# Kernel optimization log

Measured on AMD Instinct MI355X. Metric: run time of the kernel, lower is better.

## Reference

```python
import jax, jax.numpy as jnp
import numpy as np

B, CIN, COUT, K, H, W_SP = 16, 16, 16, 3, 384, 384


def setup_inputs() -> dict:
    key = jax.random.key(0)
    k1, k2 = jax.random.split(key)
    x = jax.random.normal(k1, (B, CIN, H, W_SP), dtype=jnp.float32)
    W = jax.random.normal(k2, (COUT, CIN, K, K), dtype=jnp.float32) * 0.05
    return {"x": x, "W": W}


def reference(x, W):
    b, cin, h, w = x.shape
    cout, _, kh, kw = W.shape
    # torch.where(x < 0, 0, 1): binary activity mask (x == 0 maps to 1)
    mask = (x >= 0).astype(x.dtype)
    # adaptive_avg_pool2d(mask, kh): h % kh == 0 and w % kw == 0, so bins are
    # exact equal-size means -> reshape + mean.  (b, cin, kh, kw)
    att = mask.reshape(b, cin, kh, h // kh, kw, w // kw).mean(axis=(3, 5))
    att = att.reshape(b, cin, kh * kw)
    att = kh * kw * jax.nn.softmax(att, axis=2) - 1.0
    att = 1.0 + jax.nn.sigmoid(att).reshape(b, cin, kh, kw)
    # per-sample modulated weights: (b, cout, cin, kh, kw); broadcast over cout
    wmod = W[None, :, :, :, :] * att[:, None, :, :, :]

    def conv_one(xi, wi):
        # xi: (cin, h, w), wi: (cout, cin, kh, kw); stride 1, padding 1 (same)
        return jax.lax.conv_general_dilated(
            xi[None], wi, window_strides=(1, 1), padding=[(1, 1), (1, 1)],
            dimension_numbers=("NCHW", "OIHW", "NCHW"))[0]

    # equivalent to the groups=b grouped-conv trick, but without materializing
    # the (1, b*cin, h, w) view
    y = jax.vmap(conv_one)(x, wmod)  # (b, cout, h, w)
    return y
```

## Files before the change

### kernel.cpp

```cpp
#include <hip/hip_runtime.h>
#include <hip/hip_bf16.h>
#include <math.h>

#define BB   16
#define CI   16
#define CO   16
#define HH   384
#define WW   384
#define HW   (HH * WW)

#define TSW 32
#define TSH 16
#define HSW 34
#define HSH 18
#define NPX (HSW * HSH)

typedef __bf16 bfx8 __attribute__((ext_vector_type(8)));
typedef float  f32x4 __attribute__((ext_vector_type(4)));

__device__ __forceinline__ uint32_t pack_bf16(float a, float b) {
  uint32_t ua = __builtin_bit_cast(uint32_t, a);
  uint32_t ub = __builtin_bit_cast(uint32_t, b);
  ua = (ua + 0x7FFFu + ((ua >> 16) & 1u)) >> 16;
  ub = (ub + 0x7FFFu + ((ub >> 16) & 1u)) >> 16;
  return ua | (ub << 16);
}

__global__ __launch_bounds__(256) void pool_kernel(
    const float* __restrict__ x, float* __restrict__ pooled) {
  const int bx = blockIdx.x;
  const int plane = bx / 9;
  const int bin = bx - plane * 9;
  const int br = (bin / 3) * 128;
  const int bc4 = (bin % 3) * 32;
  const float4* xp = (const float4*)(x + (size_t)plane * HW);
  const int tid = threadIdx.x;

  int cnt = 0;
#pragma unroll
  for (int k = 0; k < 16; ++k) {
    const int idx = tid + k * 256;
    const int r = idx >> 5;
    const int c4 = idx & 31;
    const float4 v = xp[(size_t)(br + r) * (WW / 4) + bc4 + c4];
    cnt += (v.x >= 0.f) + (v.y >= 0.f) + (v.z >= 0.f) + (v.w >= 0.f);
  }
#pragma unroll
  for (int s = 32; s > 0; s >>= 1) cnt += __shfl_down(cnt, s);

  __shared__ int wsum[4];
  const int lane = tid & 63, wid = tid >> 6;
  if (lane == 0) wsum[wid] = cnt;
  __syncthreads();
  if (tid == 0) {
    int t = wsum[0] + wsum[1] + wsum[2] + wsum[3];
    pooled[bx] = (float)t * (1.f / 16384.f);
  }
}

__global__ __launch_bounds__(256) void att_finish(
    const float* __restrict__ pooled, float* __restrict__ att) {
  const int plane = threadIdx.x;
  float v[9];
#pragma unroll
  for (int k = 0; k < 9; ++k) v[k] = pooled[plane * 9 + k];
  float m = v[0];
#pragma unroll
  for (int k = 1; k < 9; ++k) m = fmaxf(m, v[k]);
  float e[9], s = 0.f;
#pragma unroll
  for (int k = 0; k < 9; ++k) { e[k] = expf(v[k] - m); s += e[k]; }
  const float inv = 1.f / s;
#pragma unroll
  for (int k = 0; k < 9; ++k) {
    const float a = 9.f * e[k] * inv - 1.f;
    att[plane * 9 + k] = 1.f + 1.f / (1.f + expf(-a));
  }
}

__global__ __launch_bounds__(256) void conv_kernel(
    const float* __restrict__ x, const float* __restrict__ Wt,
    const float* __restrict__ att, float* __restrict__ y) {
  const int b   = blockIdx.z;
  const int gx0 = blockIdx.x * TSW;
  const int gy0 = blockIdx.y * TSH;
  const int tid = threadIdx.x;

  __shared__ __align__(16) uint32_t sx[NPX * 8];
  __shared__ __align__(16) uint32_t sw[CO * 80];

  const float* xb = x + (size_t)b * CI * HW;

#pragma unroll
  for (int i = 0; i < 5; ++i) {
    const int idx  = tid + 256 * i;
    const int cout = idx / 80;
    const int kp   = idx - cout * 80;
    const int k0 = 2 * kp, k1 = 2 * kp + 1;
    const int p0 = k0 >> 4, ci0 = k0 & 15;
    const int p1 = k1 >> 4, ci1 = k1 & 15;
    float v0 = 0.f, v1 = 0.f;
    if (p0 < 9) v0 = Wt[(cout * CI + ci0) * 9 + p0] * att[(b * CI + ci0) * 9 + p0];
    if (p1 < 9) v1 = Wt[(cout * CI + ci1) * 9 + p1] * att[(b * CI + ci1) * 9 + p1];
    sw[cout * 80 + kp] = pack_bf16(v0, v1);
  }

#pragma unroll
  for (int it = 0; it < 3; ++it) {
    const int pix = tid + 256 * it;
    if (pix < NPX) {
      const int rr = pix / HSW;
      const int cc = pix - rr * HSW;
      const int gr = gy0 - 1 + rr;
      const int gc = gx0 - 1 + cc;
      uint32_t pk[8];
      if (((unsigned)gr < (unsigned)HH) && ((unsigned)gc < (unsigned)WW)) {
        const float* px = xb + (size_t)gr * WW + gc;
#pragma unroll
        for (int i = 0; i < 8; ++i) {
          const float v0 = px[(size_t)(2 * i) * HW];
          const float v1 = px[(size_t)(2 * i + 1) * HW];
          pk[i] = pack_bf16(v0, v1);
        }
      } else {
#pragma unroll
        for (int i = 0; i < 8; ++i) pk[i] = 0u;
      }
      const int s = (cc >> 2) & 1;
      uint32_t* dst = &sx[pix * 8];
      uint4 lo, hi;
      lo.x = pk[0]; lo.y = pk[1]; lo.z = pk[2]; lo.w = pk[3];
      hi.x = pk[4]; hi.y = pk[5]; hi.z = pk[6]; hi.w = pk[7];
      *(uint4*)(dst + 4 * s)       = lo;
      *(uint4*)(dst + 4 * (1 - s)) = hi;
    }
  }
  __syncthreads();

  const int lane = tid & 63;
  const int wv   = tid >> 6;
  const int cpix = lane & 15;
  const int h4   = lane >> 4;
  const int hB   = h4 & 1;
  const int pp   = lane >> 5;

  bfx8 aw[5];
  const char* swb = (const char*)sw;
#pragma unroll
  for (int q = 0; q < 5; ++q)
    aw[q] = *(const bfx8*)(swb + cpix * 320 + q * 64 + h4 * 16);

  int Lq[5];
#pragma unroll
  for (int q = 0; q < 5; ++q) {
    int p = 2 * q + pp;
    if (p > 8) p = 8;
    const int dy = p / 3, dx = p - 3 * dy;
    const int ccl = cpix + dx;
    const int swz = (ccl >> 2) & 1;
    Lq[q] = (dy * HSW + ccl) * 32 + 16 * (hB ^ swz);
  }

  const char* sxb = (const char*)sx;
  float* yb = y + ((size_t)b * CO + h4 * 4) * HW + (size_t)gy0 * WW + gx0 + cpix;

#pragma unroll 2
  for (int ri = 0; ri < 4; ++ri) {
    const int r = wv * 4 + ri;
    const int gbase = (r * HSW) * 32;
    f32x4 a0 = {0.f, 0.f, 0.f, 0.f};
    f32x4 a1 = {0.f, 0.f, 0.f, 0.f};
#pragma unroll
    for (int q = 0; q < 5; ++q) {
      const bfx8 b0 = *(const bfx8*)(sxb + gbase + Lq[q]);
      const bfx8 b1 = *(const bfx8*)(sxb + gbase + 512 + Lq[q]);
      a0 = __builtin_amdgcn_mfma_f32_16x16x32_bf16(aw[q], b0, a0, 0, 0, 0);
      a1 = __builtin_amdgcn_mfma_f32_16x16x32_bf16(aw[q], b1, a1, 0, 0, 0);
    }
    float* yr = yb + (size_t)r * WW;
#pragma unroll
    for (int j = 0; j < 4; ++j) {
      yr[(size_t)j * HW]      = a0[j];
      yr[(size_t)j * HW + 16] = a1[j];
    }
  }
}

extern "C" void kernel_launch(void* const* d_in, const int* in_sizes, int n_in,
                              void* d_out, int out_size, void* d_ws,
                              size_t ws_size, hipStream_t stream) {
  const float* x  = (const float*)d_in[0];
  const float* Wt = (const float*)d_in[1];
  float* y      = (float*)d_out;
  float* pooled = (float*)d_ws;
  float* att    = (float*)d_ws + 4096;

  pool_kernel<<<dim3(BB * CI * 9), dim3(256), 0, stream>>>(x, pooled);
  att_finish<<<dim3(1), dim3(256), 0, stream>>>(pooled, att);
  conv_kernel<<<dim3(WW / TSW, HH / TSH, BB), dim3(256), 0, stream>>>(
      x, Wt, att, y);
}
```

Before: 127.0 us.

## Pre-pack input into padded bf16 channel-interleaved layout fused with pooling

Adds a prep kernel that reads x once, computes the pooled activity counts with ballots and atomics, and writes a zero-padded, pixel-major bf16 copy with 16 channels per pixel. The conv kernel then fills its shared tile with direct 16-byte global-to-LDS loads, with no bounds checks or conversions. This replaces the conv's scattered per-channel scalar loads and the separate pooling pass. In exchange it adds an intermediate buffer write and read and requires a large workspace, and the old path remains as a fallback.

Result: slower. 201.9 us (+58.9%).

```diff
diff --git a/kernel.cpp b/kernel.cpp
--- a/kernel.cpp
+++ b/kernel.cpp
@@ -9,6 +9,8 @@
 #define WW   384
 #define HW   (HH * WW)
 
+#define PW 386
+
 #define TSW 32
 #define TSH 16
 #define HSW 34
@@ -26,44 +28,69 @@
   return ua | (ub << 16);
 }
 
-__global__ __launch_bounds__(256) void pool_kernel(
-    const float* __restrict__ x, float* __restrict__ pooled) {
-  const int bx = blockIdx.x;
-  const int plane = bx / 9;
-  const int bin = bx - plane * 9;
-  const int br = (bin / 3) * 128;
-  const int bc4 = (bin % 3) * 32;
-  const float4* xp = (const float4*)(x + (size_t)plane * HW);
+__device__ __forceinline__ void gl_lds16(const void* g, void* l) {
+  __builtin_amdgcn_global_load_lds(
+      (const __attribute__((address_space(1))) uint32_t*)g,
+      (__attribute__((address_space(3))) uint32_t*)l, 16, 0, 0);
+}
+
+
+__global__ __launch_bounds__(384) void prep_kernel(
+    const float* __restrict__ x, uint4* __restrict__ XP,
+    int* __restrict__ pooled) {
+  const int pr = blockIdx.x;
+  const int b  = blockIdx.y;
   const int tid = threadIdx.x;
-
+  uint4* rowp = XP + (((size_t)b * PW + pr) * PW) * 2;
+
+  if (pr == 0 || pr == PW - 1) {
+    const uint4 z = {0u, 0u, 0u, 0u};
+    if (tid < 386) { rowp[2 * tid] = z; rowp[2 * tid + 1] = z; }
+    return;
+  }
+
+  const int h = pr - 1;
+  const int w = tid;
+  const float* px = x + ((size_t)b * CI) * HW + (size_t)h * WW + w;
+
+  uint32_t pk[8];
   int cnt = 0;
-#pragma unroll
-  for (int k = 0; k < 16; ++k) {
-    const int idx = tid + k * 256;
-    const int r = idx >> 5;
-    const int c4 = idx & 31;
-    const float4 v = xp[(size_t)(br + r) * (WW / 4) + bc4 + c4];
-    cnt += (v.x >= 0.f) + (v.y >= 0.f) + (v.z >= 0.f) + (v.w >= 0.f);
-  }
-#pragma unroll
-  for (int s = 32; s > 0; s >>= 1) cnt += __shfl_down(cnt, s);
-
-  __shared__ int wsum[4];
-  const int lane = tid & 63, wid = tid >> 6;
-  if (lane == 0) wsum[wid] = cnt;
-  __syncthreads();
+  const int lane = tid & 63;
+#pragma unroll
+  for (int i = 0; i < 8; ++i) {
+    const float v0 = px[(size_t)(2 * i) * HW];
+    const float v1 = px[(size_t)(2 * i + 1) * HW];
+    pk[i] = pack_bf16(v0, v1);
+    const unsigned long long m0 = __ballot(v0 >= 0.f);
+    const unsigned long long m1 = __ballot(v1 >= 0.f);
+    if (lane == 2 * i)     cnt = (int)__popcll(m0);
+    if (lane == 2 * i + 1) cnt = (int)__popcll(m1);
+  }
+
+  uint4 lo, hi;
+  lo.x = pk[0]; lo.y = pk[1]; lo.z = pk[2]; lo.w = pk[3];
+  hi.x = pk[4]; hi.y = pk[5]; hi.z = pk[6]; hi.w = pk[7];
+  rowp[2 * (w + 1)]     = lo;
+  rowp[2 * (w + 1) + 1] = hi;
+
   if (tid == 0) {
-    int t = wsum[0] + wsum[1] + wsum[2] + wsum[3];
-    pooled[bx] = (float)t * (1.f / 16384.f);
-  }
-}
-
-__global__ __launch_bounds__(256) void att_finish(
-    const float* __restrict__ pooled, float* __restrict__ att) {
+    const uint4 z = {0u, 0u, 0u, 0u};
+    rowp[0] = z; rowp[1] = z;
+    rowp[2 * (PW - 1)] = z; rowp[2 * (PW - 1) + 1] = z;
+  }
+
+  const int bin = (h >> 7) * 3 + (w >> 7);
+  if (lane < 16)
+    atomicAdd(&pooled[((b * CI + lane) * 9) + bin], cnt);
+}
+
+__global__ __launch_bounds__(256) void att_finish_int(
+    const int* __restrict__ pooled, float* __restrict__ att) {
   const int plane = threadIdx.x;
   float v[9];
 #pragma unroll
-  for (int k = 0; k < 9; ++k) v[k] = pooled[plane * 9 + k];
+  for (int k = 0; k < 9; ++k)
+    v[k] = (float)pooled[plane * 9 + k] * (1.f / 16384.f);
   float m = v[0];
 #pragma unroll
   for (int k = 1; k < 9; ++k) m = fmaxf(m, v[k]);
@@ -78,8 +105,8 @@
   }
 }
 
-__global__ __launch_bounds__(256) void conv_kernel(
-    const float* __restrict__ x, const float* __restrict__ Wt,
+__global__ __launch_bounds__(256) void conv_fast(
+    const char* __restrict__ XPc, const float* __restrict__ Wt,
     const float* __restrict__ att, float* __restrict__ y) {
   const int b   = blockIdx.z;
   const int gx0 = blockIdx.x * TSW;
@@ -89,7 +116,22 @@
   __shared__ __align__(16) uint32_t sx[NPX * 8];
   __shared__ __align__(16) uint32_t sw[CO * 80];
 
-  const float* xb = x + (size_t)b * CI * HW;
+  const int lane = tid & 63;
+  const int wv   = tid >> 6;
+
+  const char* XPb = XPc + (size_t)b * (PW * PW * 32);
+#pragma unroll
+  for (int i = wv; i < 20; i += 4) {
+    const int chunk = i * 64 + lane;
+    const int px  = chunk >> 1;
+    const int hf  = chunk & 1;
+    const int rr  = px / HSW;
+    const int cc  = px - rr * HSW;
+    const int swz = (cc >> 2) & 1;
+    const char* src =
+        XPb + (((size_t)(gy0 + rr) * PW + (gx0 + cc)) << 5) + ((hf ^ swz) << 4);
+    if (chunk < 2 * NPX) gl_lds16(src, (char*)sx + i * 1024);
+  }
 
 #pragma unroll
   for (int i = 0; i < 5; ++i) {
@@ -104,7 +146,126 @@
     if (p1 < 9) v1 = Wt[(cout * CI + ci1) * 9 + p1] * att[(b * CI + ci1) * 9 + p1];
     sw[cout * 80 + kp] = pack_bf16(v0, v1);
   }
-
+  __syncthreads();
+
+  const int cpix = lane & 15;
+  const int h4   = lane >> 4;
+  const int hB   = h4 & 1;
+  const int pp   = lane >> 5;
+
+  bfx8 aw[5];
+  const char* swb = (const char*)sw;
+#pragma unroll
+  for (int q = 0; q < 5; ++q)
+    aw[q] = *(const bfx8*)(swb + cpix * 320 + q * 64 + h4 * 16);
+
+  int Lq[5];
+#pragma unroll
+  for (int q = 0; q < 5; ++q) {
+    int p = 2 * q + pp;
+    if (p > 8) p = 8;
+    const int dy = p / 3, dx = p - 3 * dy;
+    const int ccl = cpix + dx;
+    const int swz = (ccl >> 2) & 1;
+    Lq[q] = (dy * HSW + ccl) * 32 + 16 * (hB ^ swz);
+  }
+
+  const char* sxb = (const char*)sx;
+  float* yb = y + ((size_t)b * CO + h4 * 4) * HW + (size_t)gy0 * WW + gx0 + cpix;
+
+#pragma unroll 2
+  for (int ri = 0; ri < 4; ++ri) {
+    const int r = wv * 4 + ri;
+    const int gbase = (r * HSW) * 32;
+    f32x4 a0 = {0.f, 0.f, 0.f, 0.f};
+    f32x4 a1 = {0.f, 0.f, 0.f, 0.f};
+#pragma unroll
+    for (int q = 0; q < 5; ++q) {
+      const bfx8 b0 = *(const bfx8*)(sxb + gbase + Lq[q]);
+      const bfx8 b1 = *(const bfx8*)(sxb + gbase + 512 + Lq[q]);
+      a0 = __builtin_amdgcn_mfma_f32_16x16x32_bf16(aw[q], b0, a0, 0, 0, 0);
+      a1 = __builtin_amdgcn_mfma_f32_16x16x32_bf16(aw[q], b1, a1, 0, 0, 0);
+    }
+    float* yr = yb + (size_t)r * WW;
+#pragma unroll
+    for (int j = 0; j < 4; ++j) {
+      yr[(size_t)j * HW]      = a0[j];
+      yr[(size_t)j * HW + 16] = a1[j];
+    }
+  }
+}
+
+__global__ __launch_bounds__(256) void pool_kernel(
+    const float* __restrict__ x, float* __restrict__ pooled) {
+  const int bx = blockIdx.x;
+  const int plane = bx / 9;
+  const int bin = bx - plane * 9;
+  const int br = (bin / 3) * 128;
+  const int bc4 = (bin % 3) * 32;
+  const float4* xp = (const float4*)(x + (size_t)plane * HW);
+  const int tid = threadIdx.x;
+  int cnt = 0;
+#pragma unroll
+  for (int k = 0; k < 16; ++k) {
+    const int idx = tid + k * 256;
+    const int r = idx >> 5;
+    const int c4 = idx & 31;
+    const float4 v = xp[(size_t)(br + r) * (WW / 4) + bc4 + c4];
+    cnt += (v.x >= 0.f) + (v.y >= 0.f) + (v.z >= 0.f) + (v.w >= 0.f);
+  }
+#pragma unroll
+  for (int s = 32; s > 0; s >>= 1) cnt += __shfl_down(cnt, s);
+  __shared__ int wsum[4];
+  const int lane = tid & 63, wid = tid >> 6;
+  if (lane == 0) wsum[wid] = cnt;
+  __syncthreads();
+  if (tid == 0)
+    pooled[bx] = (float)(wsum[0] + wsum[1] + wsum[2] + wsum[3]) * (1.f / 16384.f);
+}
+
+__global__ __launch_bounds__(256) void att_finish(
+    const float* __restrict__ pooled, float* __restrict__ att) {
+  const int plane = threadIdx.x;
+  float v[9];
+#pragma unroll
+  for (int k = 0; k < 9; ++k) v[k] = pooled[plane * 9 + k];
+  float m = v[0];
+#pragma unroll
+  for (int k = 1; k < 9; ++k) m = fmaxf(m, v[k]);
+  float e[9], s = 0.f;
+#pragma unroll
+  for (int k = 0; k < 9; ++k) { e[k] = expf(v[k] - m); s += e[k]; }
+  const float inv = 1.f / s;
+#pragma unroll
+  for (int k = 0; k < 9; ++k) {
+    const float a = 9.f * e[k] * inv - 1.f;
+    att[plane * 9 + k] = 1.f + 1.f / (1.f + expf(-a));
+  }
+}
+
+__global__ __launch_bounds__(256) void conv_legacy(
+    const float* __restrict__ x, const float* __restrict__ Wt,
+    const float* __restrict__ att, float* __restrict__ y) {
+  const int b   = blockIdx.z;
+  const int gx0 = blockIdx.x * TSW;
+  const int gy0 = blockIdx.y * TSH;
+  const int tid = threadIdx.x;
+  __shared__ __align__(16) uint32_t sx[NPX * 8];
+  __shared__ __align__(16) uint32_t sw[CO * 80];
+  const float* xb = x + (size_t)b * CI * HW;
+#pragma unroll
+  for (int i = 0; i < 5; ++i) {
+    const int idx  = tid + 256 * i;
+    const int cout = idx / 80;
+    const int kp   = idx - cout * 80;
+    const int k0 = 2 * kp, k1 = 2 * kp + 1;
+    const int p0 = k0 >> 4, ci0 = k0 & 15;
+    const int p1 = k1 >> 4, ci1 = k1 & 15;
+    float v0 = 0.f, v1 = 0.f;
+    if (p0 < 9) v0 = Wt[(cout * CI + ci0) * 9 + p0] * att[(b * CI + ci0) * 9 + p0];
+    if (p1 < 9) v1 = Wt[(cout * CI + ci1) * 9 + p1] * att[(b * CI + ci1) * 9 + p1];
+    sw[cout * 80 + kp] = pack_bf16(v0, v1);
+  }
 #pragma unroll
   for (int it = 0; it < 3; ++it) {
     const int pix = tid + 256 * it;
@@ -117,11 +278,8 @@
       if (((unsigned)gr < (unsigned)HH) && ((unsigned)gc < (unsigned)WW)) {
         const float* px = xb + (size_t)gr * WW + gc;
 #pragma unroll
-        for (int i = 0; i < 8; ++i) {
-          const float v0 = px[(size_t)(2 * i) * HW];
-          const float v1 = px[(size_t)(2 * i + 1) * HW];
-          pk[i] = pack_bf16(v0, v1);
-        }
+        for (int i = 0; i < 8; ++i)
+          pk[i] = pack_bf16(px[(size_t)(2 * i) * HW], px[(size_t)(2 * i + 1) * HW]);
       } else {
 #pragma unroll
         for (int i = 0; i < 8; ++i) pk[i] = 0u;
@@ -136,20 +294,17 @@
     }
   }
   __syncthreads();
-
   const int lane = tid & 63;
   const int wv   = tid >> 6;
   const int cpix = lane & 15;
   const int h4   = lane >> 4;
   const int hB   = h4 & 1;
   const int pp   = lane >> 5;
-
   bfx8 aw[5];
   const char* swb = (const char*)sw;
 #pragma unroll
   for (int q = 0; q < 5; ++q)
     aw[q] = *(const bfx8*)(swb + cpix * 320 + q * 64 + h4 * 16);
-
   int Lq[5];
 #pragma unroll
   for (int q = 0; q < 5; ++q) {
@@ -160,10 +315,8 @@
     const int swz = (ccl >> 2) & 1;
     Lq[q] = (dy * HSW + ccl) * 32 + 16 * (hB ^ swz);
   }
-
   const char* sxb = (const char*)sx;
   float* yb = y + ((size_t)b * CO + h4 * 4) * HW + (size_t)gy0 * WW + gx0 + cpix;
-
 #pragma unroll 2
   for (int ri = 0; ri < 4; ++ri) {
     const int r = wv * 4 + ri;
@@ -191,12 +344,25 @@
                               size_t ws_size, hipStream_t stream) {
   const float* x  = (const float*)d_in[0];
   const float* Wt = (const float*)d_in[1];
-  float* y      = (float*)d_out;
-  float* pooled = (float*)d_ws;
-  float* att    = (float*)d_ws + 4096;
-
-  pool_kernel<<<dim3(BB * CI * 9), dim3(256), 0, stream>>>(x, pooled);
-  att_finish<<<dim3(1), dim3(256), 0, stream>>>(pooled, att);
-  conv_kernel<<<dim3(WW / TSW, HH / TSH, BB), dim3(256), 0, stream>>>(
-      x, Wt, att, y);
-}
+  float* y = (float*)d_out;
+  char* wsb = (char*)d_ws;
+
+  const size_t need = 65536 + (size_t)BB * PW * PW * 32;
+  if (ws_size >= need) {
+    int*   pooled = (int*)wsb;
+    float* att    = (float*)(wsb + 16384);
+    uint4* XP     = (uint4*)(wsb + 65536);
+    hipMemsetAsync(pooled, 0, BB * CI * 9 * sizeof(int), stream);
+    prep_kernel<<<dim3(PW, BB), dim3(384), 0, stream>>>(x, XP, pooled);
+    att_finish_int<<<dim3(1), dim3(256), 0, stream>>>(pooled, att);
+    conv_fast<<<dim3(WW / TSW, HH / TSH, BB), dim3(256), 0, stream>>>(
+        (const char*)XP, Wt, att, y);
+  } else {
+    float* pooled = (float*)wsb;
+    float* att    = (float*)wsb + 4096;
+    pool_kernel<<<dim3(BB * CI * 9), dim3(256), 0, stream>>>(x, pooled);
+    att_finish<<<dim3(1), dim3(256), 0, stream>>>(pooled, att);
+    conv_legacy<<<dim3(WW / TSW, HH / TSH, BB), dim3(256), 0, stream>>>(
+        x, Wt, att, y);
+  }
+}
```
